# Performance work log

Hardware: AMD Instinct MI355X
Metric: run time of the kernel (lower is better)

The kernel has to match this reference:

```python
import jax, jax.numpy as jnp
import numpy as np

B, T, HID = 2, 1024, 1024
H, DK, DV = 16, 64, 64
K = 4            # short conv kernel size
CG = 15          # CG iterations (max_cg_step_training)
EPS = 1e-5       # norm_eps


def setup_inputs() -> dict:
    key = jax.random.key(0)
    ks = jax.random.split(key, 12)
    s = 1.0 / np.sqrt(HID)
    nrm = lambda k, sh, sc: (jax.random.normal(k, sh, jnp.float32) * sc)
    hidden_states = nrm(ks[0], (B, T, HID), 1.0)
    Wq = nrm(ks[1], (HID, HID), s)
    Wk = nrm(ks[2], (HID, HID), s)
    Wv = nrm(ks[3], (HID, HID), s)
    Wa = nrm(ks[4], (HID, H), s)
    Wb = nrm(ks[5], (HID, H), s)
    bb = jnp.zeros((H,), jnp.float32)
    A_log = jnp.log(jax.random.uniform(ks[6], (H,), jnp.float32, 1e-3, 16.0))
    dt = jnp.exp(jax.random.uniform(ks[7], (H,), jnp.float32) * (np.log(0.1) - np.log(0.001)) + np.log(0.001))
    dt = jnp.clip(dt, 1e-4)
    dt_bias = dt + jnp.log(-jnp.expm1(-dt))
    lam_init = float(np.log(np.exp(1.0 - 0.25) - 1.0))
    lambda_params = jnp.full((HID,), lam_init, jnp.float32)
    Wconv_q = nrm(ks[8], (HID, K), 0.3)
    Wconv_k = nrm(ks[9], (HID, K), 0.3)
    norm_w = jnp.ones((DV,), jnp.float32)
    Wo = nrm(ks[10], (HID, HID), s)
    return dict(hidden_states=hidden_states, Wq=Wq, Wk=Wk, Wv=Wv, Wa=Wa, Wb=Wb, bb=bb,
                A_log=A_log, dt_bias=dt_bias, lambda_params=lambda_params,
                Wconv_q=Wconv_q, Wconv_k=Wconv_k, norm_w=norm_w, Wo=Wo)


def _short_conv(x, w):
    # causal depthwise conv1d + silu. x: [b,t,c], w: [c,K]
    t = x.shape[1]
    xp = jnp.pad(x, ((0, 0), (K - 1, 0), (0, 0)))
    y = sum(xp[:, i:i + t, :] * w[:, i] for i in range(K))
    return jax.nn.silu(y)


def _l2norm(x):
    return x * jax.lax.rsqrt(jnp.sum(x * x, -1, keepdims=True) + 1e-6)


def _forward(hidden_states, Wq, Wk, Wv, Wa, Wb, bb, A_log, dt_bias, lambda_params, Wconv_q, Wconv_k, norm_w, Wo):
    b, t, _ = hidden_states.shape
    q = _short_conv(hidden_states @ Wq, Wconv_q)
    k = _short_conv(hidden_states @ Wk, Wconv_k)
    v = hidden_states @ Wv
    q = _l2norm(q.reshape(b, t, H, DK))
    k = _l2norm(k.reshape(b, t, H, DK))
    v = v.reshape(b, t, H, DV)
    beta = jax.nn.sigmoid(hidden_states @ Wb + bb)                         # [b,t,h]
    g = -jnp.exp(A_log) * jax.nn.softplus(hidden_states @ Wa + dt_bias)    # [b,t,h]
    lamb = jax.nn.softplus(lambda_params).reshape(H, DK) + 0.25            # [h,dk]

    def cg_solve(Hkk, rhs):
        # solve (Hkk + diag(lamb)) x = rhs, fixed-iteration CG, batched over [b,h]
        mv = lambda p: jnp.einsum('bhij,bhj->bhi', Hkk, p) + lamb * p
        x = jnp.zeros_like(rhs)
        r = rhs
        p = r
        rs = jnp.sum(r * r, -1, keepdims=True)
        for _ in range(CG):
            Ap = mv(p)
            alpha = rs / (jnp.sum(p * Ap, -1, keepdims=True) + 1e-12)
            x = x + alpha * p
            r = r - alpha * Ap
            rs_new = jnp.sum(r * r, -1, keepdims=True)
            p = r + (rs_new / (rs + 1e-12)) * p
            rs = rs_new
        return x

    def step(carry, inp):
        Hkk, Hkv = carry
        qt, kt, vt, gt, bt = inp
        decay = jnp.exp(gt)[..., None, None]
        w = bt[..., None, None]
        Hkk = decay * Hkk + w * (kt[..., :, None] * kt[..., None, :])
        Hkv = decay * Hkv + w * (kt[..., :, None] * vt[..., None, :])
        x = cg_solve(Hkk, qt)
        o = jnp.einsum('bhi,bhij->bhj', x, Hkv)
        return (Hkk, Hkv), o

    qT = q.transpose(1, 0, 2, 3)
    kT = k.transpose(1, 0, 2, 3)
    vT = v.transpose(1, 0, 2, 3)
    gT = g.transpose(1, 0, 2)
    bT = beta.transpose(1, 0, 2)
    Hkk0 = jnp.zeros((b, H, DK, DK), hidden_states.dtype)
    Hkv0 = jnp.zeros((b, H, DK, DV), hidden_states.dtype)
    _, oT = jax.lax.scan(jax.checkpoint(step), (Hkk0, Hkv0), (qT, kT, vT, gT, bT))
    o = oT.transpose(1, 0, 2, 3)                                           # [b,t,h,dv]
    o = o * jax.lax.rsqrt(jnp.mean(o * o, -1, keepdims=True) + EPS) * norm_w
    return o.reshape(b, t, H * DV) @ Wo


def reference(hidden_states, Wq, Wk, Wv, Wa, Wb, bb, A_log, dt_bias, lambda_params, Wconv_q, Wconv_k, norm_w, Wo):
    return _forward(hidden_states, Wq, Wk, Wv, Wa, Wb, bb, A_log, dt_bias, lambda_params, Wconv_q, Wconv_k, norm_w, Wo)
```

## Files before the change

### kernel.cpp

```cpp
#include <hip/hip_runtime.h>
#include <hip/hip_bf16.h>
#include <stdint.h>

#define T_LEN 1024
#define HIDN  1024
#define NH    16
#define DKV   64
#define KCONV 4
#define CG_IT 15
#define CC    32
#define NC    (T_LEN / CC)
#define PAD   68

typedef __attribute__((ext_vector_type(8))) short          bf16x8;
typedef __attribute__((ext_vector_type(8))) unsigned short u16x8;
typedef __attribute__((ext_vector_type(4))) unsigned short u16x4;
typedef __attribute__((ext_vector_type(4))) float          f32x4;

__device__ __forceinline__ float softplusf(float x) {
    return x > 20.f ? x : log1pf(expf(x));
}
__device__ __forceinline__ unsigned short f2bf(float x) {
    __hip_bfloat16 b = __float2bfloat16(x);
    return *reinterpret_cast<unsigned short*>(&b);
}
__device__ __forceinline__ bf16x8 pack8(float4 a, float4 b) {
    union { bf16x8 v; unsigned short u[8]; } r;
    r.u[0] = f2bf(a.x); r.u[1] = f2bf(a.y); r.u[2] = f2bf(a.z); r.u[3] = f2bf(a.w);
    r.u[4] = f2bf(b.x); r.u[5] = f2bf(b.y); r.u[6] = f2bf(b.z); r.u[7] = f2bf(b.w);
    return r.v;
}

__global__ __launch_bounds__(256) void prep(const float* __restrict__ hidden,
                                            const float* __restrict__ Wq,
                                            const float* __restrict__ Wk,
                                            const float* __restrict__ Wv,
                                            const float* __restrict__ Wo,
                                            unsigned short* __restrict__ hidden_bf,
                                            unsigned short* __restrict__ WqkvT,
                                            unsigned short* __restrict__ WoT)
{
    __shared__ unsigned short sT[64][68];
    int blk = blockIdx.x;
    int tid = threadIdx.x;
    if (blk < 2048) {
        int i = blk * 256 + tid;
        float4 v = *reinterpret_cast<const float4*>(hidden + (size_t)i * 4);
        u16x4 o;
        o.x = f2bf(v.x); o.y = f2bf(v.y); o.z = f2bf(v.z); o.w = f2bf(v.w);
        *reinterpret_cast<u16x4*>(hidden_bf + (size_t)i * 4) = o;
        return;
    }
    int r = blk - 2048;
    int m = r >> 8;
    int local = r & 255;
    int n0 = (local & 15) * 64, k0 = (local >> 4) * 64;
    const float* W = (m == 0) ? Wq : (m == 1) ? Wk : (m == 2) ? Wv : Wo;
    unsigned short* WT = (m < 3) ? (WqkvT + (size_t)m * HIDN * HIDN) : WoT;

    int rr = tid >> 4, cc4 = (tid & 15) * 4;
#pragma unroll
    for (int p = 0; p < 4; p++) {
        int rw = p * 16 + rr;
        float4 v = *reinterpret_cast<const float4*>(&W[(size_t)(k0 + rw) * HIDN + n0 + cc4]);
        sT[cc4 + 0][rw] = f2bf(v.x);
        sT[cc4 + 1][rw] = f2bf(v.y);
        sT[cc4 + 2][rw] = f2bf(v.z);
        sT[cc4 + 3][rw] = f2bf(v.w);
    }
    __syncthreads();
#pragma unroll
    for (int p = 0; p < 4; p++) {
        int rw = p * 16 + rr;
        u16x4 v = *reinterpret_cast<const u16x4*>(&sT[rw][cc4]);
        *reinterpret_cast<u16x4*>(&WT[(size_t)(n0 + rw) * HIDN + k0 + cc4]) = v;
    }
}

__global__ __launch_bounds__(256) void gemm_bf16(const unsigned short* __restrict__ A,
                                                 const unsigned short* __restrict__ Bt,
                                                 float* __restrict__ C,
                                                 int M, int N, int K)
{
    __shared__ unsigned short sA[64][40];
    __shared__ unsigned short sB[64][40];
    const int tid = threadIdx.x;
    const int bm = blockIdx.y * 64, bn = blockIdx.x * 64;
    const int w = tid >> 6, lane = tid & 63;
    const int l16 = lane & 15, quad = lane >> 4;
    const int lrow = tid >> 2, lk = (tid & 3) * 8;

    f32x4 acc[4];
#pragma unroll
    for (int f = 0; f < 4; f++) acc[f] = (f32x4){0.f, 0.f, 0.f, 0.f};

    const size_t arow = (size_t)(bm + lrow) * K;
    const size_t brow = (size_t)(bn + lrow) * K;

    for (int k0 = 0; k0 < K; k0 += 32) {
        u16x8 av = *reinterpret_cast<const u16x8*>(A + arow + k0 + lk);
        u16x8 bv = *reinterpret_cast<const u16x8*>(Bt + brow + k0 + lk);
        *reinterpret_cast<u16x8*>(&sA[lrow][lk]) = av;
        *reinterpret_cast<u16x8*>(&sB[lrow][lk]) = bv;
        __syncthreads();

        bf16x8 aF = *reinterpret_cast<const bf16x8*>(&sA[w * 16 + l16][quad * 8]);
#pragma unroll
        for (int f = 0; f < 4; f++) {
            bf16x8 bF = *reinterpret_cast<const bf16x8*>(&sB[f * 16 + l16][quad * 8]);
            acc[f] = __builtin_amdgcn_mfma_f32_16x16x32_bf16(aF, bF, acc[f], 0, 0, 0);
        }
        __syncthreads();
    }

#pragma unroll
    for (int f = 0; f < 4; f++) {
#pragma unroll
        for (int i = 0; i < 4; i++) {
            int m = bm + w * 16 + quad * 4 + i;
            C[(size_t)m * N + bn + f * 16 + l16] = acc[f][i];
        }
    }
}

__global__ __launch_bounds__(256) void gemm_qkv128(const unsigned short* __restrict__ A,
                                                   const unsigned short* __restrict__ Bt,
                                                   float* __restrict__ C)
{
    const int K = 1024;
    __shared__ unsigned short sA[128][40];
    __shared__ unsigned short sB[128][40];
    const int tid = threadIdx.x;
    const int bm = blockIdx.y * 128;
    const int bn = blockIdx.x * 128;
    const int w = tid >> 6, lane = tid & 63;
    const int l16 = lane & 15, quad = lane >> 4;
    const int wm = (w >> 1) * 64, wn = (w & 1) * 64;
    const int lrow = tid >> 1, lk = (tid & 1) * 16;

    f32x4 acc[4][4];
#pragma unroll
    for (int i = 0; i < 4; i++)
#pragma unroll
        for (int f = 0; f < 4; f++) acc[i][f] = (f32x4){0.f, 0.f, 0.f, 0.f};

    const size_t arow = (size_t)(bm + lrow) * K + lk;
    const size_t brow = (size_t)(bn + lrow) * K + lk;

    for (int k0 = 0; k0 < K; k0 += 32) {
        u16x8 a0 = *reinterpret_cast<const u16x8*>(A + arow + k0);
        u16x8 a1 = *reinterpret_cast<const u16x8*>(A + arow + k0 + 8);
        u16x8 b0 = *reinterpret_cast<const u16x8*>(Bt + brow + k0);
        u16x8 b1 = *reinterpret_cast<const u16x8*>(Bt + brow + k0 + 8);
        *reinterpret_cast<u16x8*>(&sA[lrow][lk])     = a0;
        *reinterpret_cast<u16x8*>(&sA[lrow][lk + 8]) = a1;
        *reinterpret_cast<u16x8*>(&sB[lrow][lk])     = b0;
        *reinterpret_cast<u16x8*>(&sB[lrow][lk + 8]) = b1;
        __syncthreads();

        bf16x8 af[4], bf[4];
#pragma unroll
        for (int i = 0; i < 4; i++)
            af[i] = *reinterpret_cast<const bf16x8*>(&sA[wm + 16 * i + l16][8 * quad]);
#pragma unroll
        for (int f = 0; f < 4; f++)
            bf[f] = *reinterpret_cast<const bf16x8*>(&sB[wn + 16 * f + l16][8 * quad]);
#pragma unroll
        for (int i = 0; i < 4; i++)
#pragma unroll
            for (int f = 0; f < 4; f++)
                acc[i][f] = __builtin_amdgcn_mfma_f32_16x16x32_bf16(af[i], bf[f], acc[i][f], 0, 0, 0);
        __syncthreads();
    }

#pragma unroll
    for (int i = 0; i < 4; i++) {
#pragma unroll
        for (int f = 0; f < 4; f++) {
            int ncol = bn + wn + 16 * f + l16;
            int mat = ncol >> 10, nc = ncol & 1023;
            float* Cb = C + (size_t)mat * (2048u * 1024u) + nc;
            int mrow = bm + wm + 16 * i + 4 * quad;
#pragma unroll
            for (int reg = 0; reg < 4; reg++)
                Cb[(size_t)(mrow + reg) * 1024] = acc[i][f][reg];
        }
    }
}

__global__ __launch_bounds__(256) void proj_gb(const float* __restrict__ hidden,
                                               const float* __restrict__ Wa,
                                               const float* __restrict__ Wb,
                                               const float* __restrict__ bb,
                                               const float* __restrict__ A_log,
                                               const float* __restrict__ dt_bias,
                                               float* __restrict__ g_out,
                                               float* __restrict__ beta_out)
{
    int wvid = threadIdx.x >> 6, lane = threadIdx.x & 63;
    int row = blockIdx.x * 4 + wvid;
    const float* hr = hidden + (size_t)row * HIDN + 16 * lane;
    const float* war = Wa + (size_t)(16 * lane) * NH;
    const float* wbr = Wb + (size_t)(16 * lane) * NH;

    float da[16], db[16];
#pragma unroll
    for (int h = 0; h < 16; h++) { da[h] = 0.f; db[h] = 0.f; }

#pragma unroll
    for (int j = 0; j < 16; j += 4) {
        float4 xv = *reinterpret_cast<const float4*>(hr + j);
        float xs[4] = {xv.x, xv.y, xv.z, xv.w};
#pragma unroll
        for (int e = 0; e < 4; e++) {
            int i = j + e;
            float x = xs[e];
            const float4* wa4 = reinterpret_cast<const float4*>(war + i * NH);
            const float4* wb4 = reinterpret_cast<const float4*>(wbr + i * NH);
#pragma unroll
            for (int q = 0; q < 4; q++) {
                float4 wa = wa4[q], wb = wb4[q];
                da[q * 4 + 0] += x * wa.x; da[q * 4 + 1] += x * wa.y;
                da[q * 4 + 2] += x * wa.z; da[q * 4 + 3] += x * wa.w;
                db[q * 4 + 0] += x * wb.x; db[q * 4 + 1] += x * wb.y;
                db[q * 4 + 2] += x * wb.z; db[q * 4 + 3] += x * wb.w;
            }
        }
    }
#pragma unroll
    for (int m = 1; m < 64; m <<= 1) {
#pragma unroll
        for (int h = 0; h < 16; h++) {
            da[h] += __shfl_xor(da[h], m);
            db[h] += __shfl_xor(db[h], m);
        }
    }
    float dah = 0.f, dbh = 0.f;
#pragma unroll
    for (int h = 0; h < 16; h++) {
        bool sel = (lane == h);
        dah = sel ? da[h] : dah;
        dbh = sel ? db[h] : dbh;
    }
    if (lane < 16) {
        float sp = softplusf(dah + dt_bias[lane]);
        g_out[row * NH + lane]    = -expf(A_log[lane]) * sp;
        beta_out[row * NH + lane] = 1.f / (1.f + expf(-(dbh + bb[lane])));
    }
}

__global__ __launch_bounds__(1024) void cumsum_g(const float* __restrict__ g_in,
                                                 const float* __restrict__ beta_in,
                                                 float* __restrict__ G_out,
                                                 float* __restrict__ betaT)
{
    __shared__ float s[1024];
    int bh = blockIdx.x;
    int b = bh >> 4, h = bh & 15;
    int t = threadIdx.x;
    size_t src = ((size_t)(b * T_LEN) + t) * NH + h;
    s[t] = g_in[src];
    float bt = beta_in[src];
    __syncthreads();
    for (int off = 1; off < 1024; off <<= 1) {
        float tmp = (t >= off) ? s[t - off] : 0.f;
        __syncthreads();
        s[t] += tmp;
        __syncthreads();
    }
    G_out[(size_t)bh * T_LEN + t] = s[t];
    betaT[(size_t)bh * T_LEN + t] = bt;
}

__global__ __launch_bounds__(256) void conv_silu_l2(const float* __restrict__ pre,
                                                    const float* __restrict__ Wc,
                                                    float* __restrict__ out)
{
    int gid = blockIdx.x * 4 + (threadIdx.x >> 6);
    int lane = threadIdx.x & 63;
    int h = gid & 15;
    int t = (gid >> 4) & (T_LEN - 1);
    int b = gid >> 14;
    int c = h * DKV + lane;
    float acc = 0.f;
#pragma unroll
    for (int i = 0; i < KCONV; i++) {
        int ts = t - (KCONV - 1) + i;
        if (ts >= 0)
            acc += pre[((size_t)(b * T_LEN) + ts) * HIDN + c] * Wc[c * KCONV + i];
    }
    float y = acc / (1.f + expf(-acc));
    float ss = y * y;
#pragma unroll
    for (int m = 1; m < 64; m <<= 1) ss += __shfl_xor(ss, m);
    out[((size_t)(b * T_LEN) + t) * HIDN + c] = y * rsqrtf(ss + 1e-6f);
}

__global__ __launch_bounds__(256) void chunk_local(const float* __restrict__ kbuf,
                                                   const float* __restrict__ vbuf,
                                                   const float* __restrict__ G,
                                                   const float* __restrict__ betaT,
                                                   float* __restrict__ Akk,
                                                   float* __restrict__ AkvT)
{
    __shared__ float sK[CC][PAD];
    __shared__ float sV[CC][PAD];
    __shared__ float sW[CC];
    int bid = blockIdx.x;
    int half = bid & 1;
    int cidx = bid >> 1;
    int chunk = cidx & (NC - 1), bh = cidx >> 5;
    int b = bh >> 4, h = bh & 15;
    int tid = threadIdx.x;
    int i = half * 32 + (tid >> 3);
    int j0 = (tid & 7) * 8;
    int ls = tid >> 3, ld = (tid & 7) * 8;
    int t0 = chunk * CC;

    {
        size_t ga = (((size_t)(b * T_LEN) + t0 + ls) * NH + h) * 64 + ld;
        *reinterpret_cast<float4*>(&sK[ls][ld])     = *reinterpret_cast<const float4*>(&kbuf[ga]);
        *reinterpret_cast<float4*>(&sK[ls][ld + 4]) = *reinterpret_cast<const float4*>(&kbuf[ga + 4]);
        *reinterpret_cast<float4*>(&sV[ls][ld])     = *reinterpret_cast<const float4*>(&vbuf[ga]);
        *reinterpret_cast<float4*>(&sV[ls][ld + 4]) = *reinterpret_cast<const float4*>(&vbuf[ga + 4]);
        if (tid < CC) {
            float gv = G[(size_t)bh * T_LEN + t0 + tid];
            float bv = betaT[(size_t)bh * T_LEN + t0 + tid];
            float gend = __shfl(gv, 31);
            sW[tid] = expf(gend - gv) * bv;
        }
    }
    __syncthreads();

    float akk[8], akv[8];
#pragma unroll
    for (int j = 0; j < 8; j++) { akk[j] = 0.f; akv[j] = 0.f; }
#pragma unroll 4
    for (int s = 0; s < CC; s++) {
        float wk = sW[s] * sK[s][i];
        float wv = sW[s] * sV[s][i];
        float4 ka = *reinterpret_cast<const float4*>(&sK[s][j0]);
        float4 kb = *reinterpret_cast<const float4*>(&sK[s][j0 + 4]);
        akk[0] += wk * ka.x; akk[1] += wk * ka.y; akk[2] += wk * ka.z; akk[3] += wk * ka.w;
        akk[4] += wk * kb.x; akk[5] += wk * kb.y; akk[6] += wk * kb.z; akk[7] += wk * kb.w;
        akv[0] += wv * ka.x; akv[1] += wv * ka.y; akv[2] += wv * ka.z; akv[3] += wv * ka.w;
        akv[4] += wv * kb.x; akv[5] += wv * kb.y; akv[6] += wv * kb.z; akv[7] += wv * kb.w;
    }
    size_t ob = ((size_t)cidx * 64 + i) * 64 + j0;
    *reinterpret_cast<float4*>(&Akk[ob])      = make_float4(akk[0], akk[1], akk[2], akk[3]);
    *reinterpret_cast<float4*>(&Akk[ob + 4])  = make_float4(akk[4], akk[5], akk[6], akk[7]);
    *reinterpret_cast<float4*>(&AkvT[ob])     = make_float4(akv[0], akv[1], akv[2], akv[3]);
    *reinterpret_cast<float4*>(&AkvT[ob + 4]) = make_float4(akv[4], akv[5], akv[6], akv[7]);
}

__global__ __launch_bounds__(256) void chunk_prefix(const float* __restrict__ Akk,
                                                    float* __restrict__ HkvT,
                                                    const float* __restrict__ G,
                                                    unsigned short* __restrict__ Hkk_bf)
{
    __shared__ float sDec[NC];
    int blk = blockIdx.x;
    int bh = blk >> 3, sub = blk & 7;
    int tid = threadIdx.x;
    if (tid < NC)
        sDec[tid] = (tid > 0)
            ? expf(G[(size_t)bh * T_LEN + tid * CC + CC - 1] - G[(size_t)bh * T_LEN + tid * CC - 1])
            : 1.f;
    __syncthreads();
    int flat = sub * 256 + tid;
    int mat = flat >> 10, e4 = flat & 1023;
    float4 state = make_float4(0.f, 0.f, 0.f, 0.f);
    if (mat == 0) {
        const float* src = Akk + (size_t)bh * NC * 4096 + (size_t)e4 * 4;
        unsigned short* dst = Hkk_bf + (size_t)bh * NC * 4096 + (size_t)e4 * 4;
#pragma unroll 1
        for (int c = 0; c < NC; c++) {
            float4 a = *reinterpret_cast<const float4*>(src + (size_t)c * 4096);
            u16x4 o;
            o.x = f2bf(state.x); o.y = f2bf(state.y); o.z = f2bf(state.z); o.w = f2bf(state.w);
            *reinterpret_cast<u16x4*>(dst + (size_t)c * 4096) = o;
            float d = sDec[c];
            state.x = d * state.x + a.x;
            state.y = d * state.y + a.y;
            state.z = d * state.z + a.z;
            state.w = d * state.w + a.w;
        }
    } else {
        float* base = HkvT + (size_t)bh * NC * 4096 + (size_t)e4 * 4;
#pragma unroll 1
        for (int c = 0; c < NC; c++) {
            float4* p = reinterpret_cast<float4*>(base + (size_t)c * 4096);
            float4 a = *p;
            *p = state;
            float d = sDec[c];
            state.x = d * state.x + a.x;
            state.y = d * state.y + a.y;
            state.z = d * state.z + a.z;
            state.w = d * state.w + a.w;
        }
    }
}

__global__ __launch_bounds__(256, 2) void scan_mfma(
    const float* __restrict__ qbuf, const float* __restrict__ kbuf,
    const float* __restrict__ vbuf, const float* __restrict__ G,
    const float* __restrict__ betaT, const unsigned short* __restrict__ Hkk_bf,
    const float* __restrict__ HkvT0, const float* __restrict__ lambda_p,
    const float* __restrict__ norm_w, unsigned short* __restrict__ obf)
{
    __shared__ __align__(16) unsigned short sP[4][16][72];
    __shared__ __align__(16) unsigned short sM[4][16][40];

    const int tid = threadIdx.x;
    const int wv = tid >> 6, lane = tid & 63;
    const int quad = lane >> 4, l16 = lane & 15;
    const int W = blockIdx.x * 4 + wv;
    const int half = W & 1;
    const int cidx = W >> 1;
    const int bh = cidx >> 5, chunk = cidx & 31;
    const int b = bh >> 4, h = bh & 15;
    const int t0 = chunk * CC;
    const int rbofs = 16 * half + 4 * quad;
    unsigned short (*sPw)[72] = sP[wv];
    unsigned short (*sMw)[40] = sM[wv];

    const size_t rbase = ((size_t)(b * T_LEN + t0) * NH + h) * 64;
    const float* Gb = G + (size_t)bh * T_LEN + t0;
    const float* Bb = betaT + (size_t)bh * T_LEN + t0;
    const float Gprev = (chunk > 0) ? Gb[-1] : 0.f;

    float Gt[4], et[4];
#pragma unroll
    for (int reg = 0; reg < 4; reg++) {
        float g = Gb[rbofs + reg];
        Gt[reg] = g;
        et[reg] = expf(g - Gprev);
    }
    float Co[2][4];
#pragma unroll
    for (int sn = 0; sn < 2; sn++) {
        int s = 16 * sn + l16;
        float Gs = Gb[s], bts = Bb[s];
#pragma unroll
        for (int reg = 0; reg < 4; reg++) {
            int t = rbofs + reg;
            Co[sn][reg] = (s <= t) ? expf(Gt[reg] - Gs) * bts : 0.f;
        }
    }
    float lam[4], nw[4];
#pragma unroll
    for (int f = 0; f < 4; f++) {
        lam[f] = softplusf(lambda_p[h * 64 + 16 * f + l16]) + 0.25f;
        nw[f]  = norm_w[16 * f + l16];
    }

    bf16x8 Kb[2][2];
#pragma unroll
    for (int sn = 0; sn < 2; sn++) {
        const float* kr = kbuf + rbase + (size_t)(16 * sn + l16) * 1024;
#pragma unroll
        for (int ks = 0; ks < 2; ks++) {
            float4 a = *reinterpret_cast<const float4*>(kr + 8 * quad + 32 * ks);
            float4 c = *reinterpret_cast<const float4*>(kr + 8 * quad + 32 * ks + 4);
            Kb[sn][ks] = pack8(a, c);
        }
    }
    bf16x8 KTb[4];
#pragma unroll
    for (int f = 0; f < 4; f++) {
        union { bf16x8 v; unsigned short u[8]; } r;
#pragma unroll
        for (int j = 0; j < 8; j++)
            r.u[j] = f2bf(kbuf[rbase + (size_t)(8 * quad + j) * 1024 + 16 * f + l16]);
        KTb[f] = r.v;
    }
    const size_t hbase = ((size_t)(bh * NC) + chunk) * 4096;
    bf16x8 Hb[4][2];
#pragma unroll
    for (int f = 0; f < 4; f++) {
        const unsigned short* hr = Hkk_bf + hbase + (size_t)(16 * f + l16) * 64;
#pragma unroll
        for (int ks = 0; ks < 2; ks++)
            Hb[f][ks] = *reinterpret_cast<const bf16x8*>(hr + 8 * quad + 32 * ks);
    }

    f32x4 X[4], R[4], P[4];
    float rs8[4];
#pragma unroll
    for (int reg = 0; reg < 4; reg++) rs8[reg] = 0.f;
#pragma unroll
    for (int f = 0; f < 4; f++) {
#pragma unroll
        for (int reg = 0; reg < 4; reg++) {
            float q = qbuf[rbase + (size_t)(rbofs + reg) * 1024 + 16 * f + l16];
            P[f][reg] = q; R[f][reg] = q; X[f][reg] = 0.f;
            rs8[reg] += q * q;
        }
    }
#pragma unroll
    for (int reg = 0; reg < 4; reg++) {
        float v = rs8[reg];
        v += __shfl_xor(v, 1); v += __shfl_xor(v, 2);
        v += __shfl_xor(v, 4); v += __shfl_xor(v, 8);
        rs8[reg] = v;
    }

    const f32x4 zero4 = {0.f, 0.f, 0.f, 0.f};

#pragma unroll 1
    for (int it = 0; it < CG_IT; it++) {
#pragma unroll
        for (int reg = 0; reg < 4; reg++)
#pragma unroll
            for (int f = 0; f < 4; f++)
                sPw[4 * quad + reg][16 * f + l16] = f2bf(P[f][reg]);
        __threadfence_block();
        bf16x8 Pa[2];
#pragma unroll
        for (int ks = 0; ks < 2; ks++)
            Pa[ks] = *reinterpret_cast<const bf16x8*>(&sPw[l16][8 * quad + 32 * ks]);
        f32x4 D[2];
#pragma unroll
        for (int sn = 0; sn < 2; sn++) {
            f32x4 d = __builtin_amdgcn_mfma_f32_16x16x32_bf16(Pa[0], Kb[sn][0], zero4, 0, 0, 0);
            D[sn] = __builtin_amdgcn_mfma_f32_16x16x32_bf16(Pa[1], Kb[sn][1], d, 0, 0, 0);
        }
#pragma unroll
        for (int sn = 0; sn < 2; sn++)
#pragma unroll
            for (int reg = 0; reg < 4; reg++)
                sMw[4 * quad + reg][16 * sn + l16] = f2bf(Co[sn][reg] * D[sn][reg]);
        __threadfence_block();
        bf16x8 Ma = *reinterpret_cast<const bf16x8*>(&sMw[l16][8 * quad]);
        f32x4 AP[4], A2[4];
#pragma unroll
        for (int f = 0; f < 4; f++) {
            AP[f] = __builtin_amdgcn_mfma_f32_16x16x32_bf16(Ma, KTb[f], zero4, 0, 0, 0);
            f32x4 a = __builtin_amdgcn_mfma_f32_16x16x32_bf16(Pa[0], Hb[f][0], zero4, 0, 0, 0);
            A2[f] = __builtin_amdgcn_mfma_f32_16x16x32_bf16(Pa[1], Hb[f][1], a, 0, 0, 0);
        }
#pragma unroll
        for (int f = 0; f < 4; f++)
#pragma unroll
            for (int reg = 0; reg < 4; reg++)
                AP[f][reg] = lam[f] * P[f][reg] + AP[f][reg] + et[reg] * A2[f][reg];
        float alpha[4], rsn[4];
#pragma unroll
        for (int reg = 0; reg < 4; reg++) {
            float s = 0.f;
#pragma unroll
            for (int f = 0; f < 4; f++) s += P[f][reg] * AP[f][reg];
            s += __shfl_xor(s, 1); s += __shfl_xor(s, 2);
            s += __shfl_xor(s, 4); s += __shfl_xor(s, 8);
            alpha[reg] = rs8[reg] / (s + 1e-12f);
            rsn[reg] = 0.f;
        }
#pragma unroll
        for (int f = 0; f < 4; f++)
#pragma unroll
            for (int reg = 0; reg < 4; reg++) {
                X[f][reg] += alpha[reg] * P[f][reg];
                float rv = R[f][reg] - alpha[reg] * AP[f][reg];
                R[f][reg] = rv;
                rsn[reg] += rv * rv;
            }
#pragma unroll
        for (int reg = 0; reg < 4; reg++) {
            float v = rsn[reg];
            v += __shfl_xor(v, 1); v += __shfl_xor(v, 2);
            v += __shfl_xor(v, 4); v += __shfl_xor(v, 8);
            float btac = v / (rs8[reg] + 1e-12f);
            rs8[reg] = v;
#pragma unroll
            for (int f = 0; f < 4; f++)
                P[f][reg] = R[f][reg] + btac * P[f][reg];
        }
    }

#pragma unroll
    for (int reg = 0; reg < 4; reg++)
#pragma unroll
        for (int f = 0; f < 4; f++)
            sPw[4 * quad + reg][16 * f + l16] = f2bf(X[f][reg]);
    __threadfence_block();
    bf16x8 Xa[2];
#pragma unroll
    for (int ks = 0; ks < 2; ks++)
        Xa[ks] = *reinterpret_cast<const bf16x8*>(&sPw[l16][8 * quad + 32 * ks]);
    f32x4 Do[2];
#pragma unroll
    for (int sn = 0; sn < 2; sn++) {
        f32x4 d = __builtin_amdgcn_mfma_f32_16x16x32_bf16(Xa[0], Kb[sn][0], zero4, 0, 0, 0);
        Do[sn] = __builtin_amdgcn_mfma_f32_16x16x32_bf16(Xa[1], Kb[sn][1], d, 0, 0, 0);
    }
#pragma unroll
    for (int sn = 0; sn < 2; sn++)
#pragma unroll
        for (int reg = 0; reg < 4; reg++)
            sMw[4 * quad + reg][16 * sn + l16] = f2bf(Co[sn][reg] * Do[sn][reg]);
    __threadfence_block();
    bf16x8 Mo = *reinterpret_cast<const bf16x8*>(&sMw[l16][8 * quad]);
    bf16x8 Vb[4];
#pragma unroll
    for (int f = 0; f < 4; f++) {
        union { bf16x8 v; unsigned short u[8]; } r;
#pragma unroll
        for (int j = 0; j < 8; j++)
            r.u[j] = f2bf(vbuf[rbase + (size_t)(8 * quad + j) * 1024 + 16 * f + l16]);
        Vb[f] = r.v;
    }
    bf16x8 Hvb[4][2];
#pragma unroll
    for (int f = 0; f < 4; f++) {
        const float* hr = HkvT0 + hbase + (size_t)(16 * f + l16) * 64;
#pragma unroll
        for (int ks = 0; ks < 2; ks++) {
            float4 a = *reinterpret_cast<const float4*>(hr + 8 * quad + 32 * ks);
            float4 c = *reinterpret_cast<const float4*>(hr + 8 * quad + 32 * ks + 4);
            Hvb[f][ks] = pack8(a, c);
        }
    }
    f32x4 O[4];
#pragma unroll
    for (int f = 0; f < 4; f++) {
        f32x4 o1 = __builtin_amdgcn_mfma_f32_16x16x32_bf16(Mo, Vb[f], zero4, 0, 0, 0);
        f32x4 o2 = __builtin_amdgcn_mfma_f32_16x16x32_bf16(Xa[0], Hvb[f][0], zero4, 0, 0, 0);
        o2 = __builtin_amdgcn_mfma_f32_16x16x32_bf16(Xa[1], Hvb[f][1], o2, 0, 0, 0);
#pragma unroll
        for (int reg = 0; reg < 4; reg++)
            O[f][reg] = o1[reg] + et[reg] * o2[reg];
    }
#pragma unroll
    for (int reg = 0; reg < 4; reg++) {
        float s = 0.f;
#pragma unroll
        for (int f = 0; f < 4; f++) s += O[f][reg] * O[f][reg];
        s += __shfl_xor(s, 1); s += __shfl_xor(s, 2);
        s += __shfl_xor(s, 4); s += __shfl_xor(s, 8);
        float scale = rsqrtf(s * (1.f / 64.f) + 1e-5f);
        size_t orow = rbase + (size_t)(rbofs + reg) * 1024;
#pragma unroll
        for (int f = 0; f < 4; f++)
            obf[orow + 16 * f + l16] = f2bf(O[f][reg] * scale * nw[f]);
    }
}

extern "C" void kernel_launch(void* const* d_in, const int* in_sizes, int n_in,
                              void* d_out, int out_size, void* d_ws, size_t ws_size,
                              hipStream_t stream)
{
    const float* hidden   = (const float*)d_in[0];
    const float* Wq       = (const float*)d_in[1];
    const float* Wk       = (const float*)d_in[2];
    const float* Wv       = (const float*)d_in[3];
    const float* Wa       = (const float*)d_in[4];
    const float* Wb       = (const float*)d_in[5];
    const float* bb       = (const float*)d_in[6];
    const float* A_log    = (const float*)d_in[7];
    const float* dt_bias  = (const float*)d_in[8];
    const float* lambda_p = (const float*)d_in[9];
    const float* Wconv_q  = (const float*)d_in[10];
    const float* Wconv_k  = (const float*)d_in[11];
    const float* norm_w   = (const float*)d_in[12];
    const float* Wo       = (const float*)d_in[13];
    float* out = (float*)d_out;

    float* ws = (float*)d_ws;
    const size_t SZ_BIG = (size_t)2 * T_LEN * HIDN;
    float* qpre = ws;
    float* kpre = qpre + SZ_BIG;
    float* vbuf = kpre + SZ_BIG;
    float* qbuf = vbuf + SZ_BIG;
    float* kbuf = qbuf + SZ_BIG;
    float* gbuf = kbuf + SZ_BIG;
    float* bbuf = gbuf + 32768;
    float* Gbuf = bbuf + 32768;
    float* btT  = Gbuf + 32768;
    float* Hkk0 = btT + 32768;
    float* HkvT0 = Hkk0 + (size_t)32 * NC * 4096;
    unsigned short* WoT = (unsigned short*)(HkvT0 + (size_t)32 * NC * 4096);

    unsigned short* hidden_bf = (unsigned short*)HkvT0;
    unsigned short* WqkvT = (unsigned short*)Hkk0;
    unsigned short* obuf_bf = (unsigned short*)kpre;
    unsigned short* Hkk_bf = (unsigned short*)qpre;

    const int M = 2 * T_LEN;

    prep<<<3072, 256, 0, stream>>>(hidden, Wq, Wk, Wv, Wo, hidden_bf, WqkvT, WoT);

    dim3 gq(3 * HIDN / 128, M / 128);
    gemm_qkv128<<<gq, 256, 0, stream>>>(hidden_bf, WqkvT, qpre);
    proj_gb<<<M / 4, 256, 0, stream>>>(hidden, Wa, Wb, bb, A_log, dt_bias, gbuf, bbuf);
    cumsum_g<<<32, 1024, 0, stream>>>(gbuf, bbuf, Gbuf, btT);
    conv_silu_l2<<<M * NH / 4, 256, 0, stream>>>(qpre, Wconv_q, qbuf);
    conv_silu_l2<<<M * NH / 4, 256, 0, stream>>>(kpre, Wconv_k, kbuf);
    chunk_local<<<2048, 256, 0, stream>>>(kbuf, vbuf, Gbuf, btT, Hkk0, HkvT0);
    chunk_prefix<<<256, 256, 0, stream>>>(Hkk0, HkvT0, Gbuf, Hkk_bf);
    scan_mfma<<<512, 256, 0, stream>>>(qbuf, kbuf, vbuf, Gbuf, btT, Hkk_bf, HkvT0,
                                       lambda_p, norm_w, obuf_bf);
    dim3 gg(HIDN / 64, M / 64);
    gemm_bf16<<<gg, 256, 0, stream>>>(obuf_bf, WoT, out, M, HIDN, HIDN);
}
```

Measured before the change: 269.5 us.

## Merge small kernels, rewrite cumsum as wave scan, batch chunk_prefix loads

Folds the g/beta projection into the prep kernel and merges the two conv_silu_l2 launches into one grid, which removes launches and lets independent work share one grid. The cumsum kernel moves from a 1024-thread shared-memory Hillis-Steele scan with many barriers to a 256-thread version: four elements per thread, a wave shuffle scan, and one cross-wave combine. chunk_prefix now loads four chunks ahead before the serial recurrence, so load latency is exposed less often. The work is unchanged, and a few extra registers are used in chunk_prefix.

```diff
diff --git a/kernel.cpp b/kernel.cpp
--- a/kernel.cpp
+++ b/kernel.cpp
@@ -31,14 +31,21 @@
     return r.v;
 }
 
-__global__ __launch_bounds__(256) void prep(const float* __restrict__ hidden,
-                                            const float* __restrict__ Wq,
-                                            const float* __restrict__ Wk,
-                                            const float* __restrict__ Wv,
-                                            const float* __restrict__ Wo,
-                                            unsigned short* __restrict__ hidden_bf,
-                                            unsigned short* __restrict__ WqkvT,
-                                            unsigned short* __restrict__ WoT)
+__global__ __launch_bounds__(256) void prep_proj(const float* __restrict__ hidden,
+                                                 const float* __restrict__ Wq,
+                                                 const float* __restrict__ Wk,
+                                                 const float* __restrict__ Wv,
+                                                 const float* __restrict__ Wo,
+                                                 const float* __restrict__ Wa,
+                                                 const float* __restrict__ Wb,
+                                                 const float* __restrict__ bb,
+                                                 const float* __restrict__ A_log,
+                                                 const float* __restrict__ dt_bias,
+                                                 unsigned short* __restrict__ hidden_bf,
+                                                 unsigned short* __restrict__ WqkvT,
+                                                 unsigned short* __restrict__ WoT,
+                                                 float* __restrict__ g_out,
+                                                 float* __restrict__ beta_out)
 {
     __shared__ unsigned short sT[64][68];
     int blk = blockIdx.x;
@@ -51,29 +58,82 @@
         *reinterpret_cast<u16x4*>(hidden_bf + (size_t)i * 4) = o;
         return;
     }
-    int r = blk - 2048;
-    int m = r >> 8;
-    int local = r & 255;
-    int n0 = (local & 15) * 64, k0 = (local >> 4) * 64;
-    const float* W = (m == 0) ? Wq : (m == 1) ? Wk : (m == 2) ? Wv : Wo;
-    unsigned short* WT = (m < 3) ? (WqkvT + (size_t)m * HIDN * HIDN) : WoT;
-
-    int rr = tid >> 4, cc4 = (tid & 15) * 4;
-#pragma unroll
-    for (int p = 0; p < 4; p++) {
-        int rw = p * 16 + rr;
-        float4 v = *reinterpret_cast<const float4*>(&W[(size_t)(k0 + rw) * HIDN + n0 + cc4]);
-        sT[cc4 + 0][rw] = f2bf(v.x);
-        sT[cc4 + 1][rw] = f2bf(v.y);
-        sT[cc4 + 2][rw] = f2bf(v.z);
-        sT[cc4 + 3][rw] = f2bf(v.w);
-    }
-    __syncthreads();
-#pragma unroll
-    for (int p = 0; p < 4; p++) {
-        int rw = p * 16 + rr;
-        u16x4 v = *reinterpret_cast<const u16x4*>(&sT[rw][cc4]);
-        *reinterpret_cast<u16x4*>(&WT[(size_t)(n0 + rw) * HIDN + k0 + cc4]) = v;
+    if (blk < 3072) {
+        int r = blk - 2048;
+        int m = r >> 8;
+        int local = r & 255;
+        int n0 = (local & 15) * 64, k0 = (local >> 4) * 64;
+        const float* W = (m == 0) ? Wq : (m == 1) ? Wk : (m == 2) ? Wv : Wo;
+        unsigned short* WT = (m < 3) ? (WqkvT + (size_t)m * HIDN * HIDN) : WoT;
+
+        int rr = tid >> 4, cc4 = (tid & 15) * 4;
+#pragma unroll
+        for (int p = 0; p < 4; p++) {
+            int rw = p * 16 + rr;
+            float4 v = *reinterpret_cast<const float4*>(&W[(size_t)(k0 + rw) * HIDN + n0 + cc4]);
+            sT[cc4 + 0][rw] = f2bf(v.x);
+            sT[cc4 + 1][rw] = f2bf(v.y);
+            sT[cc4 + 2][rw] = f2bf(v.z);
+            sT[cc4 + 3][rw] = f2bf(v.w);
+        }
+        __syncthreads();
+#pragma unroll
+        for (int p = 0; p < 4; p++) {
+            int rw = p * 16 + rr;
+            u16x4 v = *reinterpret_cast<const u16x4*>(&sT[rw][cc4]);
+            *reinterpret_cast<u16x4*>(&WT[(size_t)(n0 + rw) * HIDN + k0 + cc4]) = v;
+        }
+        return;
+    }
+    int wvid = tid >> 6, lane = tid & 63;
+    int row = (blk - 3072) * 4 + wvid;
+    const float* hr = hidden + (size_t)row * HIDN + 16 * lane;
+    const float* war = Wa + (size_t)(16 * lane) * NH;
+    const float* wbr = Wb + (size_t)(16 * lane) * NH;
+
+    float da[16], db[16];
+#pragma unroll
+    for (int h = 0; h < 16; h++) { da[h] = 0.f; db[h] = 0.f; }
+
+#pragma unroll
+    for (int j = 0; j < 16; j += 4) {
+        float4 xv = *reinterpret_cast<const float4*>(hr + j);
+        float xs[4] = {xv.x, xv.y, xv.z, xv.w};
+#pragma unroll
+        for (int e = 0; e < 4; e++) {
+            int i = j + e;
+            float x = xs[e];
+            const float4* wa4 = reinterpret_cast<const float4*>(war + i * NH);
+            const float4* wb4 = reinterpret_cast<const float4*>(wbr + i * NH);
+#pragma unroll
+            for (int q = 0; q < 4; q++) {
+                float4 wa = wa4[q], wb = wb4[q];
+                da[q * 4 + 0] += x * wa.x; da[q * 4 + 1] += x * wa.y;
+                da[q * 4 + 2] += x * wa.z; da[q * 4 + 3] += x * wa.w;
+                db[q * 4 + 0] += x * wb.x; db[q * 4 + 1] += x * wb.y;
+                db[q * 4 + 2] += x * wb.z; db[q * 4 + 3] += x * wb.w;
+            }
+        }
+    }
+#pragma unroll
+    for (int m = 1; m < 64; m <<= 1) {
+#pragma unroll
+        for (int h = 0; h < 16; h++) {
+            da[h] += __shfl_xor(da[h], m);
+            db[h] += __shfl_xor(db[h], m);
+        }
+    }
+    float dah = 0.f, dbh = 0.f;
+#pragma unroll
+    for (int h = 0; h < 16; h++) {
+        bool sel = (lane == h);
+        dah = sel ? da[h] : dah;
+        dbh = sel ? db[h] : dbh;
+    }
+    if (lane < 16) {
+        float sp = softplusf(dah + dt_bias[lane]);
+        g_out[row * NH + lane]    = -expf(A_log[lane]) * sp;
+        beta_out[row * NH + lane] = 1.f / (1.f + expf(-(dbh + bb[lane])));
     }
 }
 
@@ -188,95 +248,55 @@
     }
 }
 
-__global__ __launch_bounds__(256) void proj_gb(const float* __restrict__ hidden,
-                                               const float* __restrict__ Wa,
-                                               const float* __restrict__ Wb,
-                                               const float* __restrict__ bb,
-                                               const float* __restrict__ A_log,
-                                               const float* __restrict__ dt_bias,
-                                               float* __restrict__ g_out,
-                                               float* __restrict__ beta_out)
-{
-    int wvid = threadIdx.x >> 6, lane = threadIdx.x & 63;
-    int row = blockIdx.x * 4 + wvid;
-    const float* hr = hidden + (size_t)row * HIDN + 16 * lane;
-    const float* war = Wa + (size_t)(16 * lane) * NH;
-    const float* wbr = Wb + (size_t)(16 * lane) * NH;
-
-    float da[16], db[16];
-#pragma unroll
-    for (int h = 0; h < 16; h++) { da[h] = 0.f; db[h] = 0.f; }
-
-#pragma unroll
-    for (int j = 0; j < 16; j += 4) {
-        float4 xv = *reinterpret_cast<const float4*>(hr + j);
-        float xs[4] = {xv.x, xv.y, xv.z, xv.w};
-#pragma unroll
-        for (int e = 0; e < 4; e++) {
-            int i = j + e;
-            float x = xs[e];
-            const float4* wa4 = reinterpret_cast<const float4*>(war + i * NH);
-            const float4* wb4 = reinterpret_cast<const float4*>(wbr + i * NH);
-#pragma unroll
-            for (int q = 0; q < 4; q++) {
-                float4 wa = wa4[q], wb = wb4[q];
-                da[q * 4 + 0] += x * wa.x; da[q * 4 + 1] += x * wa.y;
-                da[q * 4 + 2] += x * wa.z; da[q * 4 + 3] += x * wa.w;
-                db[q * 4 + 0] += x * wb.x; db[q * 4 + 1] += x * wb.y;
-                db[q * 4 + 2] += x * wb.z; db[q * 4 + 3] += x * wb.w;
-            }
-        }
-    }
-#pragma unroll
-    for (int m = 1; m < 64; m <<= 1) {
-#pragma unroll
-        for (int h = 0; h < 16; h++) {
-            da[h] += __shfl_xor(da[h], m);
-            db[h] += __shfl_xor(db[h], m);
-        }
-    }
-    float dah = 0.f, dbh = 0.f;
-#pragma unroll
-    for (int h = 0; h < 16; h++) {
-        bool sel = (lane == h);
-        dah = sel ? da[h] : dah;
-        dbh = sel ? db[h] : dbh;
-    }
-    if (lane < 16) {
-        float sp = softplusf(dah + dt_bias[lane]);
-        g_out[row * NH + lane]    = -expf(A_log[lane]) * sp;
-        beta_out[row * NH + lane] = 1.f / (1.f + expf(-(dbh + bb[lane])));
-    }
-}
-
-__global__ __launch_bounds__(1024) void cumsum_g(const float* __restrict__ g_in,
-                                                 const float* __restrict__ beta_in,
-                                                 float* __restrict__ G_out,
-                                                 float* __restrict__ betaT)
-{
-    __shared__ float s[1024];
+__global__ __launch_bounds__(256) void cumsum_g(const float* __restrict__ g_in,
+                                                const float* __restrict__ beta_in,
+                                                float* __restrict__ G_out,
+                                                float* __restrict__ betaT)
+{
+    __shared__ float wtot[4];
     int bh = blockIdx.x;
     int b = bh >> 4, h = bh & 15;
-    int t = threadIdx.x;
-    size_t src = ((size_t)(b * T_LEN) + t) * NH + h;
-    s[t] = g_in[src];
-    float bt = beta_in[src];
+    int tid = threadIdx.x;
+    int wv = tid >> 6, lane = tid & 63;
+    int t4 = tid * 4;
+    size_t src = ((size_t)(b * T_LEN) + t4) * NH + h;
+    float g0 = g_in[src], g1 = g_in[src + NH], g2 = g_in[src + 2 * NH], g3 = g_in[src + 3 * NH];
+    float b0 = beta_in[src], b1 = beta_in[src + NH], b2 = beta_in[src + 2 * NH], b3 = beta_in[src + 3 * NH];
+    float c1 = g0 + g1, c2 = c1 + g2, c3 = c2 + g3;
+    float x = c3;
+#pragma unroll
+    for (int off = 1; off < 64; off <<= 1) {
+        float y = __shfl_up(x, off);
+        if (lane >= off) x += y;
+    }
+    float base = x - c3;
+    if (lane == 63) wtot[wv] = x;
     __syncthreads();
-    for (int off = 1; off < 1024; off <<= 1) {
-        float tmp = (t >= off) ? s[t - off] : 0.f;
-        __syncthreads();
-        s[t] += tmp;
-        __syncthreads();
-    }
-    G_out[(size_t)bh * T_LEN + t] = s[t];
-    betaT[(size_t)bh * T_LEN + t] = bt;
-}
-
-__global__ __launch_bounds__(256) void conv_silu_l2(const float* __restrict__ pre,
-                                                    const float* __restrict__ Wc,
-                                                    float* __restrict__ out)
-{
-    int gid = blockIdx.x * 4 + (threadIdx.x >> 6);
+    float woff = 0.f;
+#pragma unroll
+    for (int q = 0; q < 4; q++) woff += (q < wv) ? wtot[q] : 0.f;
+    base += woff;
+    size_t dst = (size_t)bh * T_LEN + t4;
+    G_out[dst]     = base + g0;
+    G_out[dst + 1] = base + c1;
+    G_out[dst + 2] = base + c2;
+    G_out[dst + 3] = base + c3;
+    betaT[dst] = b0; betaT[dst + 1] = b1; betaT[dst + 2] = b2; betaT[dst + 3] = b3;
+}
+
+__global__ __launch_bounds__(256) void conv_silu_l2(const float* __restrict__ qpre,
+                                                    const float* __restrict__ kpre,
+                                                    const float* __restrict__ Wcq,
+                                                    const float* __restrict__ Wck,
+                                                    float* __restrict__ qbuf,
+                                                    float* __restrict__ kbuf)
+{
+    int gidAll = blockIdx.x * 4 + (threadIdx.x >> 6);
+    int which = gidAll >> 15;
+    int gid = gidAll & 32767;
+    const float* pre = which ? kpre : qpre;
+    const float* Wc  = which ? Wck : Wcq;
+    float* out       = which ? kbuf : qbuf;
     int lane = threadIdx.x & 63;
     int h = gid & 15;
     int t = (gid >> 4) & (T_LEN - 1);
@@ -374,29 +394,40 @@
         const float* src = Akk + (size_t)bh * NC * 4096 + (size_t)e4 * 4;
         unsigned short* dst = Hkk_bf + (size_t)bh * NC * 4096 + (size_t)e4 * 4;
 #pragma unroll 1
-        for (int c = 0; c < NC; c++) {
-            float4 a = *reinterpret_cast<const float4*>(src + (size_t)c * 4096);
-            u16x4 o;
-            o.x = f2bf(state.x); o.y = f2bf(state.y); o.z = f2bf(state.z); o.w = f2bf(state.w);
-            *reinterpret_cast<u16x4*>(dst + (size_t)c * 4096) = o;
-            float d = sDec[c];
-            state.x = d * state.x + a.x;
-            state.y = d * state.y + a.y;
-            state.z = d * state.z + a.z;
-            state.w = d * state.w + a.w;
+        for (int c0 = 0; c0 < NC; c0 += 4) {
+            float4 av[4];
+#pragma unroll
+            for (int e = 0; e < 4; e++)
+                av[e] = *reinterpret_cast<const float4*>(src + (size_t)(c0 + e) * 4096);
+#pragma unroll
+            for (int e = 0; e < 4; e++) {
+                u16x4 o;
+                o.x = f2bf(state.x); o.y = f2bf(state.y); o.z = f2bf(state.z); o.w = f2bf(state.w);
+                *reinterpret_cast<u16x4*>(dst + (size_t)(c0 + e) * 4096) = o;
+                float d = sDec[c0 + e];
+                state.x = d * state.x + av[e].x;
+                state.y = d * state.y + av[e].y;
+                state.z = d * state.z + av[e].z;
+                state.w = d * state.w + av[e].w;
+            }
         }
     } else {
         float* base = HkvT + (size_t)bh * NC * 4096 + (size_t)e4 * 4;
 #pragma unroll 1
-        for (int c = 0; c < NC; c++) {
-            float4* p = reinterpret_cast<float4*>(base + (size_t)c * 4096);
-            float4 a = *p;
-            *p = state;
-            float d = sDec[c];
-            state.x = d * state.x + a.x;
-            state.y = d * state.y + a.y;
-            state.z = d * state.z + a.z;
-            state.w = d * state.w + a.w;
+        for (int c0 = 0; c0 < NC; c0 += 4) {
+            float4 av[4];
+#pragma unroll
+            for (int e = 0; e < 4; e++)
+                av[e] = *reinterpret_cast<const float4*>(base + (size_t)(c0 + e) * 4096);
+#pragma unroll
+            for (int e = 0; e < 4; e++) {
+                *reinterpret_cast<float4*>(base + (size_t)(c0 + e) * 4096) = state;
+                float d = sDec[c0 + e];
+                state.x = d * state.x + av[e].x;
+                state.y = d * state.y + av[e].y;
+                state.z = d * state.z + av[e].z;
+                state.w = d * state.w + av[e].w;
+            }
         }
     }
 }
@@ -676,28 +707,28 @@
     float* bbuf = gbuf + 32768;
     float* Gbuf = bbuf + 32768;
     float* btT  = Gbuf + 32768;
-    float* Hkk0 = btT + 32768;
-    float* HkvT0 = Hkk0 + (size_t)32 * NC * 4096;
-    unsigned short* WoT = (unsigned short*)(HkvT0 + (size_t)32 * NC * 4096);
-
-    unsigned short* hidden_bf = (unsigned short*)HkvT0;
-    unsigned short* WqkvT = (unsigned short*)Hkk0;
+    float* Akk  = btT + 32768;
+    float* AkvT = Akk + (size_t)32 * NC * 4096;
+    unsigned short* WoT = (unsigned short*)(AkvT + (size_t)32 * NC * 4096);
+
+    unsigned short* hidden_bf = (unsigned short*)AkvT;
+    unsigned short* WqkvT = (unsigned short*)Akk;
     unsigned short* obuf_bf = (unsigned short*)kpre;
     unsigned short* Hkk_bf = (unsigned short*)qpre;
 
     const int M = 2 * T_LEN;
 
-    prep<<<3072, 256, 0, stream>>>(hidden, Wq, Wk, Wv, Wo, hidden_bf, WqkvT, WoT);
+    prep_proj<<<3584, 256, 0, stream>>>(hidden, Wq, Wk, Wv, Wo, Wa, Wb, bb, A_log,
+                                        dt_bias, hidden_bf, WqkvT, WoT, gbuf, bbuf);
 
     dim3 gq(3 * HIDN / 128, M / 128);
     gemm_qkv128<<<gq, 256, 0, stream>>>(hidden_bf, WqkvT, qpre);
-    proj_gb<<<M / 4, 256, 0, stream>>>(hidden, Wa, Wb, bb, A_log, dt_bias, gbuf, bbuf);
-    cumsum_g<<<32, 1024, 0, stream>>>(gbuf, bbuf, Gbuf, btT);
-    conv_silu_l2<<<M * NH / 4, 256, 0, stream>>>(qpre, Wconv_q, qbuf);
-    conv_silu_l2<<<M * NH / 4, 256, 0, stream>>>(kpre, Wconv_k, kbuf);
-    chunk_local<<<2048, 256, 0, stream>>>(kbuf, vbuf, Gbuf, btT, Hkk0, HkvT0);
-    chunk_prefix<<<256, 256, 0, stream>>>(Hkk0, HkvT0, Gbuf, Hkk_bf);
-    scan_mfma<<<512, 256, 0, stream>>>(qbuf, kbuf, vbuf, Gbuf, btT, Hkk_bf, HkvT0,
+    cumsum_g<<<32, 256, 0, stream>>>(gbuf, bbuf, Gbuf, btT);
+    conv_silu_l2<<<2 * M * NH / 4, 256, 0, stream>>>(qpre, kpre, Wconv_q, Wconv_k,
+                                                     qbuf, kbuf);
+    chunk_local<<<2048, 256, 0, stream>>>(kbuf, vbuf, Gbuf, btT, Akk, AkvT);
+    chunk_prefix<<<256, 256, 0, stream>>>(Akk, AkvT, Gbuf, Hkk_bf);
+    scan_mfma<<<512, 256, 0, stream>>>(qbuf, kbuf, vbuf, Gbuf, btT, Hkk_bf, AkvT,
                                        lambda_p, norm_w, obuf_bf);
     dim3 gg(HIDN / 64, M / 64);
     gemm_bf16<<<gg, 256, 0, stream>>>(obuf_bf, WoT, out, M, HIDN, HIDN);
```

After: 300.7 us. +11.6%, slower.
